# Kernel tuning notes

Hardware: AMD Instinct MI355X
Metric: run time of the kernel (lower is better)

The kernel has to match this reference:

```python
import jax, jax.numpy as jnp
import numpy as np

NH = 12  # NUM_HEADING_BIN
NS = 6   # NUM_SIZE_CLUSTER
BS = 4096
NP = 4096


def _huber(error, delta):
    a = jnp.abs(error)
    q = jnp.minimum(a, delta)
    return jnp.mean(0.5 * q * q + delta * (a - q))


def _nll_from_scores(scores, labels):
    lp = jax.nn.log_softmax(scores, axis=1)
    return -jnp.mean(jnp.take_along_axis(lp, labels[:, None], axis=1))


def _corners_helper(centers, headings, sizes):
    # centers (N,3), headings (N,), sizes (N,3) -> (N,8,3)
    l, w, h = sizes[:, 0:1], sizes[:, 1:2], sizes[:, 2:3]
    sx = jnp.array([1, 1, -1, -1, 1, 1, -1, -1], dtype=sizes.dtype)
    sy = jnp.array([1, 1, 1, 1, -1, -1, -1, -1], dtype=sizes.dtype)
    sz = jnp.array([1, -1, -1, 1, 1, -1, -1, 1], dtype=sizes.dtype)
    corners = jnp.stack([(l / 2) * sx, (h / 2) * sy, (w / 2) * sz], axis=1)  # (N,3,8)
    c, s = jnp.cos(headings), jnp.sin(headings)
    z, o = jnp.zeros_like(c), jnp.ones_like(c)
    R = jnp.stack([jnp.stack([c, z, s], axis=1),
                   jnp.stack([z, o, z], axis=1),
                   jnp.stack([-s, z, c], axis=1)], axis=1)  # (N,3,3)
    out = jnp.einsum('nij,njk->nik', R, corners) + centers[:, :, None]
    return jnp.transpose(out, (0, 2, 1))


def _box3d_corners(center, heading_residuals, size_residuals, anchors):
    bs = center.shape[0]
    bins = (jnp.arange(NH) * (2.0 * np.pi / NH)).astype(center.dtype)
    headings = heading_residuals + bins[None, :]                      # (bs,NH)
    # source bug preserved: mean_sizes = anchors + size_res; sizes = mean_sizes + size_res
    sizes = anchors[None, :, :] + 2.0 * size_residuals                # (bs,NS,3)
    sizes_b = jnp.broadcast_to(sizes[:, None, :, :], (bs, NH, NS, 3)).reshape(-1, 3)
    headings_b = jnp.broadcast_to(headings[:, :, None], (bs, NH, NS)).reshape(-1)
    centers_b = jnp.broadcast_to(center[:, None, None, :], (bs, NH, NS, 3)).reshape(-1, 3)
    return _corners_helper(centers_b, headings_b, sizes_b).reshape(bs, NH, NS, 8, 3)


def setup_inputs() -> dict:
    key = jax.random.key(0)
    ks = jax.random.split(key, 16)
    return {
        'logits': jax.random.normal(ks[0], (BS, NP, 2), dtype=jnp.float32),
        'mask_label': jax.random.randint(ks[1], (BS, NP), 0, 2, dtype=jnp.int32),
        'center': jax.random.normal(ks[2], (BS, 3), dtype=jnp.float32),
        'center_label': jax.random.normal(ks[3], (BS, 3), dtype=jnp.float32),
        'stage1_center': jax.random.normal(ks[4], (BS, 3), dtype=jnp.float32),
        'heading_scores': jax.random.normal(ks[5], (BS, NH), dtype=jnp.float32),
        'heading_residual_normalized': jax.random.normal(ks[6], (BS, NH), dtype=jnp.float32),
        'heading_residual': jax.random.normal(ks[7], (BS, NH), dtype=jnp.float32),
        'heading_class_label': jax.random.randint(ks[8], (BS,), 0, NH, dtype=jnp.int32),
        'heading_residual_label': jax.random.normal(ks[9], (BS,), dtype=jnp.float32),
        'size_scores': jax.random.normal(ks[10], (BS, NS), dtype=jnp.float32),
        'size_residual_normalized': jax.random.normal(ks[11], (BS, NS, 3), dtype=jnp.float32),
        'size_residual': jax.random.normal(ks[12], (BS, NS, 3), dtype=jnp.float32),
        'size_class_label': jax.random.randint(ks[13], (BS,), 0, NS, dtype=jnp.int32),
        'size_residual_label': jax.random.normal(ks[14], (BS, 3), dtype=jnp.float32),
        'hierarchy_anchors': jax.random.uniform(ks[15], (NS, 3), dtype=jnp.float32, minval=0.5, maxval=2.0),
    }


def reference(logits, mask_label, center, center_label, stage1_center,
              heading_scores, heading_residual_normalized, heading_residual,
              heading_class_label, heading_residual_label,
              size_scores, size_residual_normalized, size_residual,
              size_class_label, size_residual_label, hierarchy_anchors,
              corner_loss_weight=10.0, box_loss_weight=1.0):
    bs = logits.shape[0]
    mask_loss = _nll_from_scores(logits.reshape(-1, 2), mask_label.reshape(-1))

    center_loss = _huber(jnp.linalg.norm(center - center_label, axis=1), 2.0)
    stage1_center_loss = _huber(jnp.linalg.norm(center - stage1_center, axis=1), 1.0)

    heading_class_loss = _nll_from_scores(heading_scores, heading_class_label)
    hcls_onehot = jax.nn.one_hot(heading_class_label, NH, dtype=jnp.float32)
    hres_norm_label = heading_residual_label / (np.pi / NH)
    hres_norm_dist = jnp.sum(heading_residual_normalized * hcls_onehot, axis=1)
    heading_residual_normalized_loss = _huber(hres_norm_dist - hres_norm_label, 1.0)

    size_class_loss = _nll_from_scores(size_scores, size_class_label)
    scls_onehot = jax.nn.one_hot(size_class_label, NS, dtype=jnp.float32)  # (bs,NS)
    pred_sres_norm = jnp.sum(size_residual_normalized * scls_onehot[:, :, None], axis=1)  # (bs,3)
    mean_size_label = jnp.sum(scls_onehot[:, :, None] * hierarchy_anchors[None], axis=1)  # (bs,3)
    sres_label_norm = size_residual_label / mean_size_label
    size_residual_normalized_loss = _huber(jnp.linalg.norm(sres_label_norm - pred_sres_norm, axis=1), 1.0)

    corners_3d = _box3d_corners(center, heading_residual, size_residual, hierarchy_anchors)  # (bs,NH,NS,8,3)
    gt_mask = hcls_onehot[:, :, None] * scls_onehot[:, None, :]  # (bs,NH,NS)
    corners_3d_pred = jnp.einsum('bhs,bhskc->bkc', gt_mask, corners_3d)  # (bs,8,3)

    bins = (jnp.arange(NH) * (2.0 * np.pi / NH)).astype(jnp.float32)
    heading_label = jnp.sum(hcls_onehot * (heading_residual_label[:, None] + bins[None]), axis=1)
    size_label = jnp.sum(scls_onehot[:, :, None] * (hierarchy_anchors[None] + size_residual_label[:, None, :]), axis=1)
    corners_3d_gt = _corners_helper(center_label, heading_label, size_label)
    corners_3d_gt_flip = _corners_helper(center_label, heading_label + np.pi, size_label)
    corners_dist = jnp.minimum(jnp.linalg.norm(corners_3d_pred - corners_3d_gt, axis=-1),
                               jnp.linalg.norm(corners_3d_pred - corners_3d_gt_flip, axis=-1))
    corners_loss = _huber(corners_dist, 1.0)

    total_loss = mask_loss + box_loss_weight * (
        center_loss + heading_class_loss + size_class_loss
        + heading_residual_normalized_loss * 20 + size_residual_normalized_loss * 20
        + stage1_center_loss + corner_loss_weight * corners_loss)
    return (total_loss, mask_loss, box_loss_weight * center_loss,
            box_loss_weight * heading_class_loss, box_loss_weight * size_class_loss,
            box_loss_weight * heading_residual_normalized_loss * 20,
            box_loss_weight * size_residual_normalized_loss * 20,
            box_loss_weight * stage1_center_loss,
            box_loss_weight * corners_loss * corner_loss_weight)
```

## Files before the change

kernel.cpp:

```cpp
#include <hip/hip_runtime.h>
#include <math.h>


constexpr int kNH = 12;
constexpr int kNS = 6;
constexpr int kBS = 4096;
constexpr int kNP = 4096;
constexpr float kPI = 3.14159265358979323846f;

constexpr int kTPB = 256;
constexpr int kMaskBlocks = 4096;
constexpr int kQPT = 4;
constexpr int kThreads = kMaskBlocks * kTPB;
static_assert(kThreads * kQPT == (kBS * kNP) / 4, "exact cover");

constexpr int kBatchBlocks = kBS / kTPB;

__device__ __forceinline__ float wave_sum(float v) {
#pragma unroll
    for (int off = 32; off > 0; off >>= 1) v += __shfl_down(v, off, 64);
    return v;
}

__device__ __forceinline__ double wave_sum_d(double v) {
#pragma unroll
    for (int off = 32; off > 0; off >>= 1) v += __shfl_down(v, off, 64);
    return v;
}

__device__ __forceinline__ float huber_el(float e, float d) {
    float a = fabsf(e);
    float q = fminf(a, d);
    return 0.5f * q * q + d * (a - q);
}

__device__ __forceinline__ float row_nll2(float s0, float s1, int lb) {
    float x = lb ? (s0 - s1) : (s1 - s0);
    return fmaxf(x, 0.f) + __logf(1.f + __expf(-fabsf(x)));
}

__global__ __launch_bounds__(256) void mask_loss_kernel(
        const float* __restrict__ logits, const int* __restrict__ labels,
        double* __restrict__ partials) {
    const int tid = blockIdx.x * kTPB + threadIdx.x;
    float4 a[kQPT], b[kQPT];
    int4 lb[kQPT];
#pragma unroll
    for (int i = 0; i < kQPT; ++i) {
        const int q = tid + i * kThreads;
        a[i] = reinterpret_cast<const float4*>(logits)[2 * q];
        b[i] = reinterpret_cast<const float4*>(logits)[2 * q + 1];
        lb[i] = reinterpret_cast<const int4*>(labels)[q];
    }
    float acc = 0.f;
#pragma unroll
    for (int i = 0; i < kQPT; ++i) {
        acc += row_nll2(a[i].x, a[i].y, lb[i].x);
        acc += row_nll2(a[i].z, a[i].w, lb[i].y);
        acc += row_nll2(b[i].x, b[i].y, lb[i].z);
        acc += row_nll2(b[i].z, b[i].w, lb[i].w);
    }
    acc = wave_sum(acc);
    __shared__ float s[4];
    if ((threadIdx.x & 63) == 0) s[threadIdx.x >> 6] = acc;
    __syncthreads();
    if (threadIdx.x == 0)
        partials[blockIdx.x] = (double)(s[0] + s[1] + s[2] + s[3]);
}

__global__ __launch_bounds__(256) void batch_loss_kernel(
        const float* __restrict__ center, const float* __restrict__ center_label,
        const float* __restrict__ stage1_center,
        const float* __restrict__ heading_scores,
        const float* __restrict__ hres_norm, const float* __restrict__ hres,
        const int* __restrict__ hcls_label, const float* __restrict__ hres_label,
        const float* __restrict__ size_scores,
        const float* __restrict__ sres_norm, const float* __restrict__ sres,
        const int* __restrict__ scls_label, const float* __restrict__ sres_label,
        const float* __restrict__ anchors, double* __restrict__ bpartials) {
    const int b = blockIdx.x * blockDim.x + threadIdx.x;
    float v[7];
#pragma unroll
    for (int j = 0; j < 7; ++j) v[j] = 0.f;
    {
        const float cx = center[3 * b], cy = center[3 * b + 1], cz = center[3 * b + 2];
        const float glx = center_label[3 * b], gly = center_label[3 * b + 1],
                    glz = center_label[3 * b + 2];
        {
            float dx = cx - glx, dy = cy - gly, dz = cz - glz;
            v[0] = huber_el(sqrtf(dx * dx + dy * dy + dz * dz), 2.0f);
            float ex = cx - stage1_center[3 * b];
            float ey = cy - stage1_center[3 * b + 1];
            float ez = cz - stage1_center[3 * b + 2];
            v[1] = huber_el(sqrtf(ex * ex + ey * ey + ez * ez), 1.0f);
        }
        const int hc = hcls_label[b];
        const int sc = scls_label[b];
        {
            float m = -1e30f;
            for (int i = 0; i < kNH; ++i) m = fmaxf(m, heading_scores[b * kNH + i]);
            float se = 0.f;
            for (int i = 0; i < kNH; ++i) se += __expf(heading_scores[b * kNH + i] - m);
            v[2] = m + __logf(se) - heading_scores[b * kNH + hc];
        }
        {
            float m = -1e30f;
            for (int i = 0; i < kNS; ++i) m = fmaxf(m, size_scores[b * kNS + i]);
            float se = 0.f;
            for (int i = 0; i < kNS; ++i) se += __expf(size_scores[b * kNS + i] - m);
            v[4] = m + __logf(se) - size_scores[b * kNS + sc];
        }
        v[3] = huber_el(hres_norm[b * kNH + hc] - hres_label[b] * ((float)kNH / kPI), 1.0f);
        const float a0 = anchors[sc * 3 + 0];
        const float a1 = anchors[sc * 3 + 1];
        const float a2 = anchors[sc * 3 + 2];
        {
            float e0 = sres_label[3 * b + 0] / a0 - sres_norm[(b * kNS + sc) * 3 + 0];
            float e1 = sres_label[3 * b + 1] / a1 - sres_norm[(b * kNS + sc) * 3 + 1];
            float e2 = sres_label[3 * b + 2] / a2 - sres_norm[(b * kNS + sc) * 3 + 2];
            v[5] = huber_el(sqrtf(e0 * e0 + e1 * e1 + e2 * e2), 1.0f);
        }
        {
            const float bin = (float)hc * (2.0f * kPI / (float)kNH);
            const float hp = hres[b * kNH + hc] + bin;
            const float hg = hres_label[b] + bin;
            const float lp = a0 + 2.f * sres[(b * kNS + sc) * 3 + 0];
            const float wp = a1 + 2.f * sres[(b * kNS + sc) * 3 + 1];
            const float tp = a2 + 2.f * sres[(b * kNS + sc) * 3 + 2];
            const float lg = a0 + sres_label[3 * b + 0];
            const float wg = a1 + sres_label[3 * b + 1];
            const float tg = a2 + sres_label[3 * b + 2];
            const float cp = cosf(hp), sp = sinf(hp);
            const float cg = cosf(hg), sg = sinf(hg);
            const float SX[8] = {1, 1, -1, -1, 1, 1, -1, -1};
            const float SY[8] = {1, 1, 1, 1, -1, -1, -1, -1};
            const float SZ[8] = {1, -1, -1, 1, 1, -1, -1, 1};
            float cl = 0.f;
#pragma unroll
            for (int k = 0; k < 8; ++k) {
                float plx = 0.5f * lp * SX[k], ply = 0.5f * tp * SY[k], plz = 0.5f * wp * SZ[k];
                float px = cp * plx + sp * plz + cx;
                float py = ply + cy;
                float pz = -sp * plx + cp * plz + cz;
                float qlx = 0.5f * lg * SX[k], qly = 0.5f * tg * SY[k], qlz = 0.5f * wg * SZ[k];
                float rx = cg * qlx + sg * qlz;
                float rz = -sg * qlx + cg * qlz;
                float dgy = py - (qly + gly);
                float d1x = px - (rx + glx), d1z = pz - (rz + glz);
                float d2x = px - (-rx + glx), d2z = pz - (-rz + glz);
                float n1 = sqrtf(d1x * d1x + dgy * dgy + d1z * d1z);
                float n2 = sqrtf(d2x * d2x + dgy * dgy + d2z * d2z);
                cl += huber_el(fminf(n1, n2), 1.0f);
            }
            v[6] = cl;
        }
    }
    __shared__ float s[4][7];
#pragma unroll
    for (int j = 0; j < 7; ++j) {
        float r = wave_sum(v[j]);
        if ((threadIdx.x & 63) == 0) s[threadIdx.x >> 6][j] = r;
    }
    __syncthreads();
    if (threadIdx.x == 0) {
#pragma unroll
        for (int j = 0; j < 7; ++j)
            bpartials[blockIdx.x * 7 + j] =
                (double)(s[0][j] + s[1][j] + s[2][j] + s[3][j]);
    }
}

__global__ __launch_bounds__(256) void finalize_kernel(
        const double* __restrict__ partials, const double* __restrict__ bpartials,
        float* __restrict__ out) {
    double acc = 0.0;
#pragma unroll
    for (int i = 0; i < kMaskBlocks / kTPB; ++i)
        acc += partials[threadIdx.x + i * kTPB];
    acc = wave_sum_d(acc);
    __shared__ double s[4];
    if ((threadIdx.x & 63) == 0) s[threadIdx.x >> 6] = acc;
    __syncthreads();
    if (threadIdx.x == 0) {
        const double mask_sum = s[0] + s[1] + s[2] + s[3];
        double bsum[7] = {0, 0, 0, 0, 0, 0, 0};
        for (int blk = 0; blk < kBatchBlocks; ++blk)
#pragma unroll
            for (int j = 0; j < 7; ++j) bsum[j] += bpartials[blk * 7 + j];
        const double inv_rows = 1.0 / ((double)kBS * (double)kNP);
        const double inv_bs = 1.0 / (double)kBS;
        float mask_l = (float)(mask_sum * inv_rows);
        float center_l = (float)(bsum[0] * inv_bs);
        float stage1_l = (float)(bsum[1] * inv_bs);
        float hclass_l = (float)(bsum[2] * inv_bs);
        float hres_l20 = (float)(bsum[3] * inv_bs * 20.0);
        float sclass_l = (float)(bsum[4] * inv_bs);
        float sres_l20 = (float)(bsum[5] * inv_bs * 20.0);
        float corners10 = (float)(bsum[6] * inv_bs * (1.0 / 8.0) * 10.0);
        float total = mask_l + center_l + hclass_l + sclass_l + hres_l20 + sres_l20 +
                      stage1_l + corners10;
        out[0] = total;
        out[1] = mask_l;
        out[2] = center_l;
        out[3] = hclass_l;
        out[4] = sclass_l;
        out[5] = hres_l20;
        out[6] = sres_l20;
        out[7] = stage1_l;
        out[8] = corners10;
    }
}

extern "C" void kernel_launch(void* const* d_in, const int* in_sizes, int n_in,
                              void* d_out, int out_size, void* d_ws, size_t ws_size,
                              hipStream_t stream) {
    const float* logits = (const float*)d_in[0];
    const int* mask_label = (const int*)d_in[1];
    const float* center = (const float*)d_in[2];
    const float* center_label = (const float*)d_in[3];
    const float* stage1_center = (const float*)d_in[4];
    const float* heading_scores = (const float*)d_in[5];
    const float* hres_norm = (const float*)d_in[6];
    const float* hres = (const float*)d_in[7];
    const int* hcls_label = (const int*)d_in[8];
    const float* hres_label = (const float*)d_in[9];
    const float* size_scores = (const float*)d_in[10];
    const float* sres_norm = (const float*)d_in[11];
    const float* sres = (const float*)d_in[12];
    const int* scls_label = (const int*)d_in[13];
    const float* sres_label = (const float*)d_in[14];
    const float* anchors = (const float*)d_in[15];

    double* partials = (double*)d_ws;
    double* bpartials = partials + kMaskBlocks;

    mask_loss_kernel<<<kMaskBlocks, kTPB, 0, stream>>>(logits, mask_label, partials);
    batch_loss_kernel<<<kBatchBlocks, kTPB, 0, stream>>>(
        center, center_label, stage1_center, heading_scores, hres_norm, hres,
        hcls_label, hres_label, size_scores, sres_norm, sres, scls_label,
        sres_label, anchors, bpartials);
    finalize_kernel<<<1, kTPB, 0, stream>>>(partials, bpartials, (float*)d_out);
}
```

Measured before the change: 45.37 us.

## Fuse mask and batch loss kernels into one launch with nontemporal loads

Merges the mask-loss and batch-loss kernels into a single grid, with the extra trailing blocks running the per-batch box loss, so one launch and its gap disappear. The mask path is rewritten to read one float4 of logits plus an int2 of labels per step, with nontemporal loads for the streamed logits, in groups of four per thread. This trades the earlier 2x float4 plus int4 access pattern for narrower label loads and adds a branch on block index. The result depends on launch overhead versus the memory-bandwidth-bound streaming of 128 MB of logits.

```diff
diff --git a/kernel.cpp b/kernel.cpp
--- a/kernel.cpp
+++ b/kernel.cpp
@@ -10,11 +10,15 @@
 
 constexpr int kTPB = 256;
 constexpr int kMaskBlocks = 4096;
-constexpr int kQPT = 4;
-constexpr int kThreads = kMaskBlocks * kTPB;
-static_assert(kThreads * kQPT == (kBS * kNP) / 4, "exact cover");
+constexpr int kF4 = (kBS * kNP) / 2;
+constexpr int kMaskThreads = kMaskBlocks * kTPB;
+constexpr int kF4PerThread = kF4 / kMaskThreads;
+static_assert(kF4PerThread * kMaskThreads == kF4, "exact cover");
 
 constexpr int kBatchBlocks = kBS / kTPB;
+constexpr int kGrid = kMaskBlocks + kBatchBlocks;
+
+typedef float vf4 __attribute__((ext_vector_type(4)));
 
 __device__ __forceinline__ float wave_sum(float v) {
 #pragma unroll
@@ -39,36 +43,8 @@
     return fmaxf(x, 0.f) + __logf(1.f + __expf(-fabsf(x)));
 }
 
-__global__ __launch_bounds__(256) void mask_loss_kernel(
-        const float* __restrict__ logits, const int* __restrict__ labels,
-        double* __restrict__ partials) {
-    const int tid = blockIdx.x * kTPB + threadIdx.x;
-    float4 a[kQPT], b[kQPT];
-    int4 lb[kQPT];
-#pragma unroll
-    for (int i = 0; i < kQPT; ++i) {
-        const int q = tid + i * kThreads;
-        a[i] = reinterpret_cast<const float4*>(logits)[2 * q];
-        b[i] = reinterpret_cast<const float4*>(logits)[2 * q + 1];
-        lb[i] = reinterpret_cast<const int4*>(labels)[q];
-    }
-    float acc = 0.f;
-#pragma unroll
-    for (int i = 0; i < kQPT; ++i) {
-        acc += row_nll2(a[i].x, a[i].y, lb[i].x);
-        acc += row_nll2(a[i].z, a[i].w, lb[i].y);
-        acc += row_nll2(b[i].x, b[i].y, lb[i].z);
-        acc += row_nll2(b[i].z, b[i].w, lb[i].w);
-    }
-    acc = wave_sum(acc);
-    __shared__ float s[4];
-    if ((threadIdx.x & 63) == 0) s[threadIdx.x >> 6] = acc;
-    __syncthreads();
-    if (threadIdx.x == 0)
-        partials[blockIdx.x] = (double)(s[0] + s[1] + s[2] + s[3]);
-}
-
-__global__ __launch_bounds__(256) void batch_loss_kernel(
+__device__ void batch_loss_body(
+        int bid,
         const float* __restrict__ center, const float* __restrict__ center_label,
         const float* __restrict__ stage1_center,
         const float* __restrict__ heading_scores,
@@ -78,7 +54,7 @@
         const float* __restrict__ sres_norm, const float* __restrict__ sres,
         const int* __restrict__ scls_label, const float* __restrict__ sres_label,
         const float* __restrict__ anchors, double* __restrict__ bpartials) {
-    const int b = blockIdx.x * blockDim.x + threadIdx.x;
+    const int b = bid * kTPB + threadIdx.x;
     float v[7];
 #pragma unroll
     for (int j = 0; j < 7; ++j) v[j] = 0.f;
@@ -165,9 +141,54 @@
     if (threadIdx.x == 0) {
 #pragma unroll
         for (int j = 0; j < 7; ++j)
-            bpartials[blockIdx.x * 7 + j] =
-                (double)(s[0][j] + s[1][j] + s[2][j] + s[3][j]);
-    }
+            bpartials[bid * 7 + j] = (double)(s[0][j] + s[1][j] + s[2][j] + s[3][j]);
+    }
+}
+
+__global__ __launch_bounds__(256) void fused_loss_kernel(
+        const float* __restrict__ logits, const int* __restrict__ labels,
+        const float* __restrict__ center, const float* __restrict__ center_label,
+        const float* __restrict__ stage1_center,
+        const float* __restrict__ heading_scores,
+        const float* __restrict__ hres_norm, const float* __restrict__ hres,
+        const int* __restrict__ hcls_label, const float* __restrict__ hres_label,
+        const float* __restrict__ size_scores,
+        const float* __restrict__ sres_norm, const float* __restrict__ sres,
+        const int* __restrict__ scls_label, const float* __restrict__ sres_label,
+        const float* __restrict__ anchors, double* __restrict__ ws) {
+    if (blockIdx.x >= (unsigned)kMaskBlocks) {
+        batch_loss_body(blockIdx.x - kMaskBlocks, center, center_label,
+                        stage1_center, heading_scores, hres_norm, hres,
+                        hcls_label, hres_label, size_scores, sres_norm, sres,
+                        scls_label, sres_label, anchors, ws + kMaskBlocks);
+        return;
+    }
+    const int tid = blockIdx.x * kTPB + threadIdx.x;
+    const vf4* __restrict__ lg4 = reinterpret_cast<const vf4*>(logits);
+    const int2* __restrict__ lb2 = reinterpret_cast<const int2*>(labels);
+    float acc = 0.f;
+#pragma unroll
+    for (int g = 0; g < kF4PerThread / 4; ++g) {
+        vf4 a[4];
+        int2 lb[4];
+#pragma unroll
+        for (int i = 0; i < 4; ++i) {
+            const int idx = tid + (g * 4 + i) * kMaskThreads;
+            a[i] = __builtin_nontemporal_load(lg4 + idx);
+            lb[i] = lb2[idx];
+        }
+#pragma unroll
+        for (int i = 0; i < 4; ++i) {
+            acc += row_nll2(a[i][0], a[i][1], lb[i].x);
+            acc += row_nll2(a[i][2], a[i][3], lb[i].y);
+        }
+    }
+    acc = wave_sum(acc);
+    __shared__ float s[4];
+    if ((threadIdx.x & 63) == 0) s[threadIdx.x >> 6] = acc;
+    __syncthreads();
+    if (threadIdx.x == 0)
+        ws[blockIdx.x] = (double)(s[0] + s[1] + s[2] + s[3]);
 }
 
 __global__ __launch_bounds__(256) void finalize_kernel(
@@ -231,13 +252,11 @@
     const float* sres_label = (const float*)d_in[14];
     const float* anchors = (const float*)d_in[15];
 
-    double* partials = (double*)d_ws;
-    double* bpartials = partials + kMaskBlocks;
-
-    mask_loss_kernel<<<kMaskBlocks, kTPB, 0, stream>>>(logits, mask_label, partials);
-    batch_loss_kernel<<<kBatchBlocks, kTPB, 0, stream>>>(
-        center, center_label, stage1_center, heading_scores, hres_norm, hres,
-        hcls_label, hres_label, size_scores, sres_norm, sres, scls_label,
-        sres_label, anchors, bpartials);
-    finalize_kernel<<<1, kTPB, 0, stream>>>(partials, bpartials, (float*)d_out);
-}
+    double* ws = (double*)d_ws;
+
+    fused_loss_kernel<<<kGrid, kTPB, 0, stream>>>(
+        logits, mask_label, center, center_label, stage1_center, heading_scores,
+        hres_norm, hres, hcls_label, hres_label, size_scores, sres_norm, sres,
+        scls_label, sres_label, anchors, ws);
+    finalize_kernel<<<1, kTPB, 0, stream>>>(ws, ws + kMaskBlocks, (float*)d_out);
+}
```

Result: faster. 43.25 us (-4.7%).
